# Performance work log

Measured on AMD Instinct MI355X. Metric: run time of the kernel, lower is better.

Reference implementation:

```python
import jax, jax.numpy as jnp
import numpy as np

B, S, D, H = 2, 4096, 512, 8
DH = D // H  # head dim = 64


def setup_inputs() -> dict:
    key = jax.random.key(0)
    ks = jax.random.split(key, 5)
    s = 1.0 / np.sqrt(D)
    return {
        "x": jax.random.normal(ks[0], (B, S, D), jnp.float32),
        "Wq": jax.random.normal(ks[1], (D, D), jnp.float32) * s,
        "bq": jnp.zeros((D,), jnp.float32),
        "Wk": jax.random.normal(ks[2], (D, D), jnp.float32) * s,
        "bk": jnp.zeros((D,), jnp.float32),
        "Wv": jax.random.normal(ks[3], (D, D), jnp.float32) * s,
        "bv": jnp.zeros((D,), jnp.float32),
        "Wo": jax.random.normal(ks[4], (D, D), jnp.float32) * s,
        "bo": jnp.zeros((D,), jnp.float32),
    }


def _split_heads(t):  # [B,S,D] -> [B,H,S,DH]
    return t.reshape(B, S, H, DH).transpose(0, 2, 1, 3)


def reference(x, Wq, bq, Wk, bk, Wv, bv, Wo, bo):
    relu = jax.nn.relu
    # linear projections with activation (keras MultiHeadAttention applies
    # the activation to all Q/K/V/output mappings)
    q = _split_heads(relu(x @ Wq + bq))
    k = _split_heads(relu(x @ Wk + bk))
    v = _split_heads(relu(x @ Wv + bv))
    # scaled dot-product attention; scale uses per-head feature dim (DH)
    e = jnp.einsum("bhqd,bhkd->bhqk", q, k) / jnp.sqrt(jnp.float32(DH))
    attn = jax.nn.softmax(e, axis=-1)  # stable max-subtract softmax
    o = jnp.einsum("bhqk,bhkd->bhqd", attn, v)
    o = o.transpose(0, 2, 1, 3).reshape(B, S, D)  # merge heads
    return relu(o @ Wo + bo)
```

## Files before the change

### kernel.cpp

```cpp
#include <hip/hip_runtime.h>
#include <stdint.h>

#define B_ 2
#define S_ 4096
#define D_ 512
#define H_ 8
#define DH_ 64
#define M_ (B_*S_)
#define LOG2E 1.4426950408889634f

typedef unsigned short u16;
typedef __bf16 bf16x8 __attribute__((ext_vector_type(8)));
typedef __bf16 bf16x4 __attribute__((ext_vector_type(4)));
typedef float f32x4 __attribute__((ext_vector_type(4)));

#if defined(__has_builtin)
#if __has_builtin(__builtin_amdgcn_exp2f)
#define EXP2(x) __builtin_amdgcn_exp2f(x)
#else
#define EXP2(x) exp2f(x)
#endif
#else
#define EXP2(x) exp2f(x)
#endif

__device__ __forceinline__ u16 f2bf(float f) {
  __bf16 b = (__bf16)f;
  return __builtin_bit_cast(u16, b);
}

__device__ __forceinline__ void gl_lds16(const void* g, void* l) {
  __builtin_amdgcn_global_load_lds(
      (__attribute__((address_space(1))) void*)(void*)g,
      (__attribute__((address_space(3))) void*)l, 16, 0, 0);
}

#define MM(a, b, c) __builtin_amdgcn_mfma_f32_16x16x32_bf16((a), (b), (c), 0, 0, 0)
#define LD8(p) (*(const bf16x8*)(p))

__global__ void k_cvt(const float* __restrict__ x, u16* __restrict__ xb, int n4) {
  int i = blockIdx.x * 256 + threadIdx.x;
  if (i < n4) {
    float4 v = ((const float4*)x)[i];
    bf16x4 o;
    o[0] = (__bf16)v.x; o[1] = (__bf16)v.y; o[2] = (__bf16)v.z; o[3] = (__bf16)v.w;
    ((bf16x4*)xb)[i] = o;
  }
}

__global__ void k_twt(const float* __restrict__ w0, const float* __restrict__ w1,
                      const float* __restrict__ w2, const float* __restrict__ w3,
                      u16* __restrict__ t0, u16* __restrict__ t1,
                      u16* __restrict__ t2, u16* __restrict__ t3) {
  __shared__ float t[32][33];
  int z = blockIdx.z;
  const float* w = z == 0 ? w0 : z == 1 ? w1 : z == 2 ? w2 : w3;
  u16* wt       = z == 0 ? t0 : z == 1 ? t1 : z == 2 ? t2 : t3;
  int n0 = blockIdx.x * 32, k0 = blockIdx.y * 32;
  int tx = threadIdx.x, ty = threadIdx.y;
  #pragma unroll
  for (int j = 0; j < 4; j++) t[ty + 8*j][tx] = w[(k0 + ty + 8*j) * D_ + n0 + tx];
  __syncthreads();
  #pragma unroll
  for (int j = 0; j < 4; j++) wt[(n0 + ty + 8*j) * D_ + k0 + tx] = f2bf(t[tx][ty + 8*j]);
}

__device__ __forceinline__
void gemm_body(const u16* __restrict__ A, const u16* __restrict__ Bt,
               const float* __restrict__ bias, void* __restrict__ out,
               float scale, int mode) {
  __shared__ __align__(16) u16 Al[128*64];
  __shared__ __align__(16) u16 Bl[128*64];
  int tid = threadIdx.x;
  int lane = tid & 63, w = tid >> 6;
  int wr = w >> 2, wc = w & 3;
  int g = lane >> 4, qi = lane & 15;
  int m0 = blockIdx.y * 128, n0 = blockIdx.x * 128;
  int swzc = ((lane & 7) ^ (lane >> 3)) * 8;
  int lr8 = lane >> 3;

  f32x4 acc[4][2] = {};

  for (int k0 = 0; k0 < D_; k0 += 64) {
    #pragma unroll
    for (int j = 0; j < 2; j++) {
      int r0 = (w*2 + j) * 8;
      gl_lds16(A  + (m0 + r0 + lr8) * D_ + k0 + swzc, &Al[r0 * 64]);
      gl_lds16(Bt + (n0 + r0 + lr8) * D_ + k0 + swzc, &Bl[r0 * 64]);
    }
    __syncthreads();
    #pragma unroll
    for (int h = 0; h < 2; h++) {
      bf16x8 a[4], bq[2];
      #pragma unroll
      for (int i = 0; i < 4; i++) {
        int row = wr*64 + i*16 + qi;
        int c = (h*4 + g) ^ (row & 7);
        a[i] = LD8(&Al[row*64 + c*8]);
      }
      #pragma unroll
      for (int jn = 0; jn < 2; jn++) {
        int row = wc*32 + jn*16 + qi;
        int c = (h*4 + g) ^ (row & 7);
        bq[jn] = LD8(&Bl[row*64 + c*8]);
      }
      #pragma unroll
      for (int i = 0; i < 4; i++)
        #pragma unroll
        for (int jn = 0; jn < 2; jn++)
          acc[i][jn] = MM(a[i], bq[jn], acc[i][jn]);
    }
    __syncthreads();
  }

  #pragma unroll
  for (int i = 0; i < 4; i++)
    #pragma unroll
    for (int jn = 0; jn < 2; jn++) {
      int col = n0 + wc*32 + jn*16 + qi;
      float bs = bias[col];
      if (mode == 1) {
        int row0 = m0 + wr*64 + i*16 + g*4;
        int bb = row0 >> 12, ss0 = row0 & (S_ - 1);
        int hh = col >> 6, dd = col & 63;
        bf16x4 pk;
        pk[0] = (__bf16)(fmaxf(acc[i][jn][0] + bs, 0.0f) * scale);
        pk[1] = (__bf16)(fmaxf(acc[i][jn][1] + bs, 0.0f) * scale);
        pk[2] = (__bf16)(fmaxf(acc[i][jn][2] + bs, 0.0f) * scale);
        pk[3] = (__bf16)(fmaxf(acc[i][jn][3] + bs, 0.0f) * scale);
        *(bf16x4*)&((u16*)out)[((bb*H_ + hh)*DH_ + dd)*S_ + ss0] = pk;
      } else {
        #pragma unroll
        for (int ii = 0; ii < 4; ii++) {
          int row = m0 + wr*64 + i*16 + g*4 + ii;
          float v = fmaxf(acc[i][jn][ii] + bs, 0.0f) * scale;
          if (mode == 2) {
            ((float*)out)[row * D_ + col] = v;
          } else {
            int bb = row >> 12, ss = row & (S_ - 1);
            int hh = col >> 6, dd = col & 63;
            ((u16*)out)[((bb*H_ + hh)*S_ + ss)*DH_ + dd] = f2bf(v);
          }
        }
      }
    }
}

__global__ __launch_bounds__(512, 2)
void k_qkv(const u16* __restrict__ A,
           const u16* __restrict__ btq, const u16* __restrict__ btk, const u16* __restrict__ btv,
           const float* __restrict__ bq, const float* __restrict__ bk, const float* __restrict__ bv,
           u16* __restrict__ q, u16* __restrict__ k, u16* __restrict__ v) {
  int z = blockIdx.z;
  if (z == 0)      gemm_body(A, btq, bq, q, 0.125f * LOG2E, 0);
  else if (z == 1) gemm_body(A, btk, bk, k, 1.0f, 0);
  else             gemm_body(A, btv, bv, v, 1.0f, 1);
}

__global__ __launch_bounds__(512, 2)
void k_go(const u16* __restrict__ A, const u16* __restrict__ bt,
          const float* __restrict__ bias, float* __restrict__ out) {
  gemm_body(A, bt, bias, out, 1.0f, 2);
}

template<int BUF, int LAST>
__device__ __forceinline__ void attn_tile(
    const u16*& kp0, const u16*& kp1, const u16*& vp0, const u16*& vp1,
    u16* (&kdst)[2][2], u16* (&vdst)[2][2],
    const u16* Kl0, const u16* Kl1, const u16* Vl0, const u16* Vl1,
    char* Pw, const int (&fo)[4][2], const int (&pwo)[4], int pr0, int pr1,
    bf16x8 aqA0, bf16x8 aqA1, bf16x8 aqB0, bf16x8 aqB1,
    f32x4 (&oA)[4], f32x4 (&oB)[4], float& lA, float& lB) {
  if (!LAST) {
    gl_lds16(kp0, kdst[BUF^1][0]);
    gl_lds16(kp1, kdst[BUF^1][1]);
    gl_lds16(vp0, vdst[BUF^1][0]);
    gl_lds16(vp1, vdst[BUF^1][1]);
    kp0 += 64*DH_; kp1 += 64*DH_; vp0 += 64; vp1 += 64;
    asm volatile("s_waitcnt vmcnt(4)" ::: "memory");
  } else {
    asm volatile("s_waitcnt vmcnt(0)" ::: "memory");
  }
  __builtin_amdgcn_s_barrier();
  __builtin_amdgcn_sched_barrier(0);
  const char* Kb = (const char*)(BUF ? Kl1 : Kl0);
  const char* Vb = (const char*)(BUF ? Vl1 : Vl0);
  const f32x4 zro = {0.f, 0.f, 0.f, 0.f};

  f32x4 sA[4], sB[4];
  #pragma unroll
  for (int kt = 0; kt < 4; kt++) {
    bf16x8 k0 = LD8(Kb + fo[kt][0]);
    bf16x8 k1 = LD8(Kb + fo[kt][1]);
    sA[kt] = MM(k1, aqA1, MM(k0, aqA0, zro));
    sB[kt] = MM(k1, aqB1, MM(k0, aqB0, zro));
  }

  float suA = 0.0f, suB = 0.0f;
  #pragma unroll
  for (int kt = 0; kt < 4; kt++) {
    float a0 = EXP2(sA[kt][0]), a1 = EXP2(sA[kt][1]);
    float a2 = EXP2(sA[kt][2]), a3 = EXP2(sA[kt][3]);
    suA += (a0+a1)+(a2+a3);
    bf16x4 pa; pa[0]=(__bf16)a0; pa[1]=(__bf16)a1; pa[2]=(__bf16)a2; pa[3]=(__bf16)a3;
    *(bf16x4*)(Pw + pwo[kt]) = pa;
    float b0 = EXP2(sB[kt][0]), b1 = EXP2(sB[kt][1]);
    float b2 = EXP2(sB[kt][2]), b3 = EXP2(sB[kt][3]);
    suB += (b0+b1)+(b2+b3);
    bf16x4 pb; pb[0]=(__bf16)b0; pb[1]=(__bf16)b1; pb[2]=(__bf16)b2; pb[3]=(__bf16)b3;
    *(bf16x4*)(Pw + 2048 + pwo[kt]) = pb;
  }
  lA += suA; lB += suB;

  __builtin_amdgcn_s_setprio(1);
  #pragma unroll
  for (int kh = 0; kh < 2; kh++) {
    bf16x8 apA = LD8(Pw + (kh ? pr1 : pr0));
    bf16x8 apB = LD8(Pw + 2048 + (kh ? pr1 : pr0));
    #pragma unroll
    for (int nt = 0; nt < 4; nt++) {
      bf16x8 vf = LD8(Vb + fo[nt][kh]);
      oA[nt] = MM(apA, vf, oA[nt]);
      oB[nt] = MM(apB, vf, oB[nt]);
    }
  }
  __builtin_amdgcn_s_setprio(0);
  __builtin_amdgcn_sched_barrier(0);
  __builtin_amdgcn_s_barrier();
}

__global__ __launch_bounds__(256, 2)
void k_attn(const u16* __restrict__ Q, const u16* __restrict__ K,
            const u16* __restrict__ Vt, u16* __restrict__ O) {
  __shared__ __align__(16) u16 Kl[2][64*64];
  __shared__ __align__(16) u16 Vl[2][64*64];
  __shared__ __align__(16) u16 Pl[4][32*64];
  const int tid = threadIdx.x;
  const int lane = tid & 63, w = tid >> 6;
  const int g = lane >> 4, qi = lane & 15, qi7 = qi & 7;

  const int bid = blockIdx.x;
  const int xcd = bid & 7, idx = bid >> 3;
  const int hb = xcd * 2 + (idx & 1);
  const int qt = idx >> 1;
  const int b = hb >> 3, h = hb & 7;

  const u16* Qh = Q  + ((b*H_ + h) * S_) * DH_;
  const u16* Kh = K  + ((b*H_ + h) * S_) * DH_;
  const u16* Vh = Vt + ((b*H_ + h) * DH_) * S_;
  const int q0 = qt*128 + w*32;

  const bf16x8 aqA0 = LD8(&Qh[(q0 + qi)*DH_ + g*8]);
  const bf16x8 aqA1 = LD8(&Qh[(q0 + qi)*DH_ + 32 + g*8]);
  const bf16x8 aqB0 = LD8(&Qh[(q0 + 16 + qi)*DH_ + g*8]);
  const bf16x8 aqB1 = LD8(&Qh[(q0 + 16 + qi)*DH_ + 32 + g*8]);

  f32x4 oA[4] = {}, oB[4] = {};
  float lA = 0.0f, lB = 0.0f;

  const int swzc = ((lane & 7) ^ (lane >> 3)) * 8;
  const int lr8 = lane >> 3;

  int fo[4][2];
  #pragma unroll
  for (int rt = 0; rt < 4; rt++)
    #pragma unroll
    for (int kh = 0; kh < 2; kh++)
      fo[rt][kh] = (rt*16 + qi)*128 + (((kh*4 + g) ^ qi7)*16);
  int pwo[4];
  #pragma unroll
  for (int kt = 0; kt < 4; kt++)
    pwo[kt] = qi*128 + (((kt*2 + (g >> 1)) ^ qi7)*16) + (g & 1)*8;
  const int pr0 = qi*128 + ((g ^ qi7)*16);
  const int pr1 = qi*128 + (((4 + g) ^ qi7)*16);
  char* Pw = (char*)Pl[w];

  const u16* kp0 = Kh + (w*16 + lr8)*DH_ + swzc;
  const u16* kp1 = kp0 + 8*DH_;
  const u16* vp0 = Vh + (w*16 + lr8)*S_ + swzc;
  const u16* vp1 = vp0 + 8*S_;
  u16* kdst[2][2];
  u16* vdst[2][2];
  #pragma unroll
  for (int bb2 = 0; bb2 < 2; bb2++)
    #pragma unroll
    for (int j = 0; j < 2; j++) {
      kdst[bb2][j] = &Kl[bb2][(w*16 + j*8)*64];
      vdst[bb2][j] = &Vl[bb2][(w*16 + j*8)*64];
    }

  gl_lds16(kp0, kdst[0][0]);
  gl_lds16(kp1, kdst[0][1]);
  gl_lds16(vp0, vdst[0][0]);
  gl_lds16(vp1, vdst[0][1]);
  kp0 += 64*DH_; kp1 += 64*DH_; vp0 += 64; vp1 += 64;

#define T(BUF, LAST) attn_tile<BUF, LAST>(kp0, kp1, vp0, vp1, kdst, vdst, \
    &Kl[0][0], &Kl[1][0], &Vl[0][0], &Vl[1][0], Pw, fo, pwo, pr0, pr1, \
    aqA0, aqA1, aqB0, aqB1, oA, oB, lA, lB)

  for (int i = 0; i < 31; ++i) {
    T(0, 0);
    T(1, 0);
  }
  T(0, 0);
  T(1, 1);
#undef T

  lA += __shfl_xor(lA, 16); lA += __shfl_xor(lA, 32);
  lB += __shfl_xor(lB, 16); lB += __shfl_xor(lB, 32);
  float rvA = 1.0f / lA, rvB = 1.0f / lB;
  float rrA[4], rrB[4];
  #pragma unroll
  for (int i = 0; i < 4; i++) {
    rrA[i] = __shfl(rvA, g*4 + i);
    rrB[i] = __shfl(rvB, g*4 + i);
  }
  #pragma unroll
  for (int ii = 0; ii < 4; ii++) {
    int rowA = q0 + g*4 + ii;
    u16* oaro = O + (b*S_ + rowA)*D_ + h*64 + qi;
    oaro[0]  = f2bf(oA[0][ii] * rrA[ii]);
    oaro[16] = f2bf(oA[1][ii] * rrA[ii]);
    oaro[32] = f2bf(oA[2][ii] * rrA[ii]);
    oaro[48] = f2bf(oA[3][ii] * rrA[ii]);
    u16* obro = oaro + 16*D_;
    obro[0]  = f2bf(oB[0][ii] * rrB[ii]);
    obro[16] = f2bf(oB[1][ii] * rrB[ii]);
    obro[32] = f2bf(oB[2][ii] * rrB[ii]);
    obro[48] = f2bf(oB[3][ii] * rrB[ii]);
  }
}

extern "C" void kernel_launch(void* const* d_in, const int* in_sizes, int n_in,
                              void* d_out, int out_size, void* d_ws, size_t ws_size,
                              hipStream_t stream) {
  (void)in_sizes; (void)n_in; (void)out_size; (void)ws_size;
  const float* x  = (const float*)d_in[0];
  const float* Wq = (const float*)d_in[1];
  const float* bq = (const float*)d_in[2];
  const float* Wk = (const float*)d_in[3];
  const float* bk = (const float*)d_in[4];
  const float* Wv = (const float*)d_in[5];
  const float* bv = (const float*)d_in[6];
  const float* Wo = (const float*)d_in[7];
  const float* bo = (const float*)d_in[8];

  char* ws = (char*)d_ws;
  u16* xb  = (u16*)ws;
  u16* wtq = (u16*)(ws + 8388608);
  u16* wtk = wtq + 512*512;
  u16* wtv = wtk + 512*512;
  u16* wto = wtv + 512*512;
  u16* Qh  = (u16*)(ws + 8388608 + 4*524288);
  u16* Kh  = Qh + M_*D_;
  u16* Vt  = Kh + M_*D_;
  u16* Ob  = xb;

  k_cvt<<<4096, 256, 0, stream>>>(x, xb, M_*D_/4);
  k_twt<<<dim3(16,16,4), dim3(32,8), 0, stream>>>(Wq, Wk, Wv, Wo, wtq, wtk, wtv, wto);
  k_qkv<<<dim3(4,64,3), 512, 0, stream>>>(xb, wtq, wtk, wtv, bq, bk, bv, Qh, Kh, Vt);
  k_attn<<<512, 256, 0, stream>>>(Qh, Kh, Vt, Ob);
  k_go<<<dim3(4,64), 512, 0, stream>>>(Ob, wto, bo, (float*)d_out);
}
```

Before: 203.7 us.

## Double-buffer GEMM LDS tiles with async prefetch and merge prep kernels

The projection GEMM now uses two LDS buffers per operand. It issues the global-to-LDS loads for the next K tile before computing the current one, using explicit vmcnt waits and raw barriers instead of syncthreads, and the K loop is unrolled into eight templated steps. LDS fragment offsets are precomputed once. Separately, the x conversion and weight transpose kernels are merged into one launch to save a kernel launch. The cost is twice the LDS use per block, which may lower occupancy, plus more hand-managed synchronisation that is easy to get wrong.

Result: faster. 199.4 us (-2.1%).

```diff
diff --git a/kernel.cpp b/kernel.cpp
--- a/kernel.cpp
+++ b/kernel.cpp
@@ -38,80 +38,124 @@
 #define MM(a, b, c) __builtin_amdgcn_mfma_f32_16x16x32_bf16((a), (b), (c), 0, 0, 0)
 #define LD8(p) (*(const bf16x8*)(p))
 
-__global__ void k_cvt(const float* __restrict__ x, u16* __restrict__ xb, int n4) {
-  int i = blockIdx.x * 256 + threadIdx.x;
-  if (i < n4) {
+__global__ void k_prep(const float* __restrict__ x, u16* __restrict__ xb,
+                       const float* __restrict__ w0, const float* __restrict__ w1,
+                       const float* __restrict__ w2, const float* __restrict__ w3,
+                       u16* __restrict__ t0, u16* __restrict__ t1,
+                       u16* __restrict__ t2, u16* __restrict__ t3) {
+  __shared__ float t[32][33];
+  int bid = blockIdx.x, tid = threadIdx.x;
+  if (bid < 4096) {
+    int i = bid * 256 + tid;
     float4 v = ((const float4*)x)[i];
     bf16x4 o;
     o[0] = (__bf16)v.x; o[1] = (__bf16)v.y; o[2] = (__bf16)v.z; o[3] = (__bf16)v.w;
     ((bf16x4*)xb)[i] = o;
-  }
-}
-
-__global__ void k_twt(const float* __restrict__ w0, const float* __restrict__ w1,
-                      const float* __restrict__ w2, const float* __restrict__ w3,
-                      u16* __restrict__ t0, u16* __restrict__ t1,
-                      u16* __restrict__ t2, u16* __restrict__ t3) {
-  __shared__ float t[32][33];
-  int z = blockIdx.z;
-  const float* w = z == 0 ? w0 : z == 1 ? w1 : z == 2 ? w2 : w3;
-  u16* wt       = z == 0 ? t0 : z == 1 ? t1 : z == 2 ? t2 : t3;
-  int n0 = blockIdx.x * 32, k0 = blockIdx.y * 32;
-  int tx = threadIdx.x, ty = threadIdx.y;
-  #pragma unroll
-  for (int j = 0; j < 4; j++) t[ty + 8*j][tx] = w[(k0 + ty + 8*j) * D_ + n0 + tx];
-  __syncthreads();
-  #pragma unroll
-  for (int j = 0; j < 4; j++) wt[(n0 + ty + 8*j) * D_ + k0 + tx] = f2bf(t[tx][ty + 8*j]);
+  } else {
+    int zb = bid - 4096;
+    int z = zb >> 8;
+    int rem = zb & 255;
+    int bx = rem & 15, by = rem >> 4;
+    const float* w = z == 0 ? w0 : z == 1 ? w1 : z == 2 ? w2 : w3;
+    u16* wt       = z == 0 ? t0 : z == 1 ? t1 : z == 2 ? t2 : t3;
+    int n0 = bx * 32, k0 = by * 32;
+    int tx = tid & 31, ty = tid >> 5;
+    #pragma unroll
+    for (int j = 0; j < 4; j++) t[ty + 8*j][tx] = w[(k0 + ty + 8*j) * D_ + n0 + tx];
+    __syncthreads();
+    #pragma unroll
+    for (int j = 0; j < 4; j++) wt[(n0 + ty + 8*j) * D_ + k0 + tx] = f2bf(t[tx][ty + 8*j]);
+  }
+}
+
+template<int BUF, int LAST>
+__device__ __forceinline__ void gemm_step(
+    const u16*& Ap0, const u16*& Ap1, const u16*& Bp0, const u16*& Bp1,
+    u16* (&Adst)[2][2], u16* (&Bdst)[2][2],
+    const u16* Al0, const u16* Al1, const u16* Bl0, const u16* Bl1,
+    const int (&afo)[2][4], const int (&bfo)[2][2], f32x4 (&acc)[4][2]) {
+  if (!LAST) {
+    gl_lds16(Ap0, Adst[BUF^1][0]);
+    gl_lds16(Ap1, Adst[BUF^1][1]);
+    gl_lds16(Bp0, Bdst[BUF^1][0]);
+    gl_lds16(Bp1, Bdst[BUF^1][1]);
+    Ap0 += 64; Ap1 += 64; Bp0 += 64; Bp1 += 64;
+    asm volatile("s_waitcnt vmcnt(4)" ::: "memory");
+  } else {
+    asm volatile("s_waitcnt vmcnt(0)" ::: "memory");
+  }
+  __builtin_amdgcn_s_barrier();
+  __builtin_amdgcn_sched_barrier(0);
+  const char* Ab = (const char*)(BUF ? Al1 : Al0);
+  const char* Bb = (const char*)(BUF ? Bl1 : Bl0);
+  #pragma unroll
+  for (int h = 0; h < 2; h++) {
+    bf16x8 a0 = LD8(Ab + afo[h][0]);
+    bf16x8 a1 = LD8(Ab + afo[h][1]);
+    bf16x8 a2 = LD8(Ab + afo[h][2]);
+    bf16x8 a3 = LD8(Ab + afo[h][3]);
+    bf16x8 b0 = LD8(Bb + bfo[h][0]);
+    bf16x8 b1 = LD8(Bb + bfo[h][1]);
+    acc[0][0] = MM(a0, b0, acc[0][0]); acc[0][1] = MM(a0, b1, acc[0][1]);
+    acc[1][0] = MM(a1, b0, acc[1][0]); acc[1][1] = MM(a1, b1, acc[1][1]);
+    acc[2][0] = MM(a2, b0, acc[2][0]); acc[2][1] = MM(a2, b1, acc[2][1]);
+    acc[3][0] = MM(a3, b0, acc[3][0]); acc[3][1] = MM(a3, b1, acc[3][1]);
+  }
+  __builtin_amdgcn_sched_barrier(0);
+  __builtin_amdgcn_s_barrier();
 }
 
 __device__ __forceinline__
 void gemm_body(const u16* __restrict__ A, const u16* __restrict__ Bt,
                const float* __restrict__ bias, void* __restrict__ out,
                float scale, int mode) {
-  __shared__ __align__(16) u16 Al[128*64];
-  __shared__ __align__(16) u16 Bl[128*64];
+  __shared__ __align__(16) u16 Al[2][128*64];
+  __shared__ __align__(16) u16 Bl[2][128*64];
   int tid = threadIdx.x;
   int lane = tid & 63, w = tid >> 6;
   int wr = w >> 2, wc = w & 3;
-  int g = lane >> 4, qi = lane & 15;
+  int g = lane >> 4, qi = lane & 15, qi7 = qi & 7;
   int m0 = blockIdx.y * 128, n0 = blockIdx.x * 128;
   int swzc = ((lane & 7) ^ (lane >> 3)) * 8;
   int lr8 = lane >> 3;
 
   f32x4 acc[4][2] = {};
 
-  for (int k0 = 0; k0 < D_; k0 += 64) {
+  int afo[2][4], bfo[2][2];
+  #pragma unroll
+  for (int h = 0; h < 2; h++) {
+    #pragma unroll
+    for (int i = 0; i < 4; i++)
+      afo[h][i] = (wr*64 + i*16 + qi)*128 + (((h*4 + g) ^ qi7)*16);
+    #pragma unroll
+    for (int jn = 0; jn < 2; jn++)
+      bfo[h][jn] = (wc*32 + jn*16 + qi)*128 + (((h*4 + g) ^ qi7)*16);
+  }
+
+  const u16* Ap0 = A  + (m0 + w*16 + lr8)*D_ + swzc;
+  const u16* Ap1 = Ap0 + 8*D_;
+  const u16* Bp0 = Bt + (n0 + w*16 + lr8)*D_ + swzc;
+  const u16* Bp1 = Bp0 + 8*D_;
+  u16* Adst[2][2];
+  u16* Bdst[2][2];
+  #pragma unroll
+  for (int bb2 = 0; bb2 < 2; bb2++)
     #pragma unroll
     for (int j = 0; j < 2; j++) {
-      int r0 = (w*2 + j) * 8;
-      gl_lds16(A  + (m0 + r0 + lr8) * D_ + k0 + swzc, &Al[r0 * 64]);
-      gl_lds16(Bt + (n0 + r0 + lr8) * D_ + k0 + swzc, &Bl[r0 * 64]);
+      Adst[bb2][j] = &Al[bb2][(w*16 + j*8)*64];
+      Bdst[bb2][j] = &Bl[bb2][(w*16 + j*8)*64];
     }
-    __syncthreads();
-    #pragma unroll
-    for (int h = 0; h < 2; h++) {
-      bf16x8 a[4], bq[2];
-      #pragma unroll
-      for (int i = 0; i < 4; i++) {
-        int row = wr*64 + i*16 + qi;
-        int c = (h*4 + g) ^ (row & 7);
-        a[i] = LD8(&Al[row*64 + c*8]);
-      }
-      #pragma unroll
-      for (int jn = 0; jn < 2; jn++) {
-        int row = wc*32 + jn*16 + qi;
-        int c = (h*4 + g) ^ (row & 7);
-        bq[jn] = LD8(&Bl[row*64 + c*8]);
-      }
-      #pragma unroll
-      for (int i = 0; i < 4; i++)
-        #pragma unroll
-        for (int jn = 0; jn < 2; jn++)
-          acc[i][jn] = MM(a[i], bq[jn], acc[i][jn]);
-    }
-    __syncthreads();
-  }
+
+  gl_lds16(Ap0, Adst[0][0]);
+  gl_lds16(Ap1, Adst[0][1]);
+  gl_lds16(Bp0, Bdst[0][0]);
+  gl_lds16(Bp1, Bdst[0][1]);
+  Ap0 += 64; Ap1 += 64; Bp0 += 64; Bp1 += 64;
+
+#define GS(BUF, LAST) gemm_step<BUF, LAST>(Ap0, Ap1, Bp0, Bp1, Adst, Bdst, \
+    Al[0], Al[1], Bl[0], Bl[1], afo, bfo, acc)
+  GS(0,0); GS(1,0); GS(0,0); GS(1,0); GS(0,0); GS(1,0); GS(0,0); GS(1,1);
+#undef GS
 
   #pragma unroll
   for (int i = 0; i < 4; i++)
@@ -357,8 +401,7 @@
   u16* Vt  = Kh + M_*D_;
   u16* Ob  = xb;
 
-  k_cvt<<<4096, 256, 0, stream>>>(x, xb, M_*D_/4);
-  k_twt<<<dim3(16,16,4), dim3(32,8), 0, stream>>>(Wq, Wk, Wv, Wo, wtq, wtk, wtv, wto);
+  k_prep<<<5120, 256, 0, stream>>>(x, xb, Wq, Wk, Wv, Wo, wtq, wtk, wtv, wto);
   k_qkv<<<dim3(4,64,3), 512, 0, stream>>>(xb, wtq, wtk, wtv, bq, bk, bv, Qh, Kh, Vt);
   k_attn<<<512, 256, 0, stream>>>(Qh, Kh, Vt, Ob);
   k_go<<<dim3(4,64), 512, 0, stream>>>(Ob, wto, bo, (float*)d_out);
```
